# Kernel tuning notes

Measured on AMD Instinct MI355X. Metric: run time of the kernel, lower is better.

Reference implementation:

```python
import jax, jax.numpy as jnp
import numpy as np

N_NODES = 100000
FEATS = 128
N_EDGES = 600000


def setup_inputs() -> dict:
    key = jax.random.key(0)
    ks = jax.random.split(key, 8)
    s = 1.0 / np.sqrt(2 * FEATS)
    s2 = 1.0 / np.sqrt(FEATS)
    return {
        "item_feats": jax.random.normal(ks[0], (N_NODES, FEATS), jnp.float32),
        "user_feats": jax.random.normal(ks[1], (N_NODES, FEATS), jnp.float32),
        "W1": jax.random.uniform(ks[2], (FEATS, 2 * FEATS), jnp.float32, -s, s),
        "b1": jax.random.uniform(ks[3], (FEATS,), jnp.float32, -s, s),
        "W2": jax.random.uniform(ks[4], (1, FEATS), jnp.float32, -s2, s2),
        "b2": jax.random.uniform(ks[5], (1,), jnp.float32, -s2, s2),
        "src_idx": jax.random.randint(ks[6], (N_EDGES,), 0, N_NODES, jnp.int64 if jax.config.jax_enable_x64 else jnp.int32),
        "dst_idx": jax.random.randint(ks[7], (N_EDGES,), 0, N_NODES, jnp.int64 if jax.config.jax_enable_x64 else jnp.int32),
    }


def reference(item_feats, user_feats, W1, b1, W2, b2, src_idx, dst_idx):
    # Per-edge gather + concat: h[e] = [item_feats[src[e]], user_feats[dst[e]]]  -> [E, 2F]
    h = jnp.concatenate([item_feats[src_idx], user_feats[dst_idx]], axis=1)
    # fc1 -> ReLU -> fc2 -> squeeze(1)  (torch Linear: y = x @ W.T + b)
    h1 = jax.nn.relu(h @ W1.T + b1)          # [E, F]
    score = (h1 @ W2.T + b2)[:, 0]           # [E]
    return score
```

## Files before the change

kernel.cpp:

```cpp
#include <hip/hip_runtime.h>
#include <hip/hip_bf16.h>

#define NFEATS 128

typedef __attribute__((ext_vector_type(8))) short bf16x8;
typedef __attribute__((ext_vector_type(4))) float f32x4;
typedef __attribute__((ext_vector_type(4))) short short4v;

__device__ inline short f2bf(float f) {
    union { float f; unsigned u; } c; c.f = f;
    unsigned u = c.u;
    return (short)((u + 0x7FFFu + ((u >> 16) & 1u)) >> 16);
}
__device__ inline float bf2f(short v) {
    union { unsigned u; float f; } c;
    c.u = ((unsigned)(unsigned short)v) << 16;
    return c.f;
}

__global__ __launch_bounds__(512) void precompute_kernel(
    const float* __restrict__ item, const float* __restrict__ user,
    const float* __restrict__ W1, const float* __restrict__ b1,
    short* __restrict__ A, short* __restrict__ B, int n_nodes)
{
    const int which = blockIdx.y;
    const float* __restrict__ X = which ? user : item;
    short* __restrict__ Out = which ? B : A;
    const int k_off4 = which ? 32 : 0;

    __shared__ short Wlds[128][136];
    const int tid = threadIdx.x;

    const float4* W4 = (const float4*)W1;
    for (int i = tid; i < 128 * 32; i += 512) {
        int j = i >> 5, c = i & 31;
        float4 w = W4[j * 64 + k_off4 + c];
        short4v p;
        p[0] = f2bf(w.x); p[1] = f2bf(w.y); p[2] = f2bf(w.z); p[3] = f2bf(w.w);
        *(short4v*)&Wlds[j][c * 4] = p;
    }
    __syncthreads();

    const int wave = tid >> 6, lane = tid & 63;
    const int r16 = lane & 15, q = lane >> 4;
    const int row_base = blockIdx.x * 256 + wave * 32;

    bf16x8 afrag[2][4];
#pragma unroll
    for (int m = 0; m < 2; ++m) {
        int row = row_base + m * 16 + r16;
        if (row >= n_nodes) row = n_nodes - 1;
        const float* xr = X + (size_t)row * NFEATS;
#pragma unroll
        for (int kk = 0; kk < 4; ++kk) {
            int k0 = kk * 32 + q * 8;
            float4 lo = *(const float4*)(xr + k0);
            float4 hi = *(const float4*)(xr + k0 + 4);
            bf16x8 f;
            f[0] = f2bf(lo.x); f[1] = f2bf(lo.y); f[2] = f2bf(lo.z); f[3] = f2bf(lo.w);
            f[4] = f2bf(hi.x); f[5] = f2bf(hi.y); f[6] = f2bf(hi.z); f[7] = f2bf(hi.w);
            afrag[m][kk] = f;
        }
    }

    f32x4 acc[2][8];
#pragma unroll
    for (int n = 0; n < 8; ++n) {
        float bv = which ? 0.f : b1[n * 16 + r16];
        f32x4 init = {bv, bv, bv, bv};
        acc[0][n] = init;
        acc[1][n] = init;
    }

#pragma unroll
    for (int n = 0; n < 8; ++n) {
#pragma unroll
        for (int kk = 0; kk < 4; ++kk) {
            bf16x8 wf = *(const bf16x8*)&Wlds[n * 16 + r16][kk * 32 + q * 8];
            acc[0][n] = __builtin_amdgcn_mfma_f32_16x16x32_bf16(afrag[0][kk], wf, acc[0][n], 0, 0, 0);
            acc[1][n] = __builtin_amdgcn_mfma_f32_16x16x32_bf16(afrag[1][kk], wf, acc[1][n], 0, 0, 0);
        }
    }

#pragma unroll
    for (int m = 0; m < 2; ++m) {
#pragma unroll
        for (int r = 0; r < 4; ++r) {
            int row = row_base + m * 16 + q * 4 + r;
            if (row < n_nodes) {
                short* orow = Out + (size_t)row * NFEATS;
#pragma unroll
                for (int n = 0; n < 8; ++n)
                    orow[n * 16 + r16] = f2bf(acc[m][n][r]);
            }
        }
    }
}

__global__ __launch_bounds__(256) void edge_kernel(
    const short* __restrict__ A, const short* __restrict__ B,
    const int* __restrict__ src, const int* __restrict__ dst,
    const float* __restrict__ W2, const float* __restrict__ b2,
    float* __restrict__ out, int n_edges)
{
    const int t = blockIdx.x * 256 + threadIdx.x;
    const int lane16 = threadIdx.x & 15;

    float w2v[8];
#pragma unroll
    for (int j = 0; j < 8; ++j) w2v[j] = W2[lane16 * 8 + j];
    const float b2v = b2[0];

    const int qw = t >> 4;
    const int nqw = (gridDim.x * 256) >> 4;

    for (int e0 = qw; e0 < n_edges; e0 += 2 * nqw) {
        const int e1 = e0 + nqw;
        const bool has1 = e1 < n_edges;

        int s0 = src[e0], d0 = dst[e0];
        int s1 = has1 ? src[e1] : s0;
        int d1 = has1 ? dst[e1] : d0;

        bf16x8 av0 = *(const bf16x8*)(A + (size_t)s0 * NFEATS + lane16 * 8);
        bf16x8 bv0 = *(const bf16x8*)(B + (size_t)d0 * NFEATS + lane16 * 8);
        bf16x8 av1 = *(const bf16x8*)(A + (size_t)s1 * NFEATS + lane16 * 8);
        bf16x8 bv1 = *(const bf16x8*)(B + (size_t)d1 * NFEATS + lane16 * 8);

        float acc0 = 0.f, acc1 = 0.f;
#pragma unroll
        for (int j = 0; j < 8; ++j) {
            float h0 = bf2f(av0[j]) + bf2f(bv0[j]);
            h0 = fmaxf(h0, 0.f);
            acc0 = fmaf(h0, w2v[j], acc0);
            float h1 = bf2f(av1[j]) + bf2f(bv1[j]);
            h1 = fmaxf(h1, 0.f);
            acc1 = fmaf(h1, w2v[j], acc1);
        }
#pragma unroll
        for (int sh = 1; sh <= 8; sh <<= 1) {
            acc0 += __shfl_xor(acc0, sh);
            acc1 += __shfl_xor(acc1, sh);
        }
        if (lane16 == 0) {
            out[e0] = acc0 + b2v;
            if (has1) out[e1] = acc1 + b2v;
        }
    }
}

extern "C" void kernel_launch(void* const* d_in, const int* in_sizes, int n_in,
                              void* d_out, int out_size, void* d_ws, size_t ws_size,
                              hipStream_t stream) {
    const float* item = (const float*)d_in[0];
    const float* user = (const float*)d_in[1];
    const float* W1   = (const float*)d_in[2];
    const float* b1   = (const float*)d_in[3];
    const float* W2   = (const float*)d_in[4];
    const float* b2   = (const float*)d_in[5];
    const int*   src  = (const int*)d_in[6];
    const int*   dst  = (const int*)d_in[7];
    float* out = (float*)d_out;

    const int n_nodes = in_sizes[0] / NFEATS;
    const int n_edges = in_sizes[6];

    short* A = (short*)d_ws;
    short* B = A + (size_t)n_nodes * NFEATS;

    const int nblk = (n_nodes + 255) / 256;
    dim3 grid(nblk, 2);
    precompute_kernel<<<grid, 512, 0, stream>>>(item, user, W1, b1, A, B, n_nodes);

    edge_kernel<<<2048, 256, 0, stream>>>(A, B, src, dst, W2, b2, out, n_edges);
}
```

Before: 89.07 us.

## Make precompute persistent with double-buffered async global-to-LDS loads

The node precompute GEMM now runs as a persistent grid of 256×2 blocks looping over 64-row tiles. Each block holds its W1 fragments in registers and prefetches the next tile of node features into a second LDS buffer with global_load_lds while it computes the current one. LDS rows are XOR-swizzled to avoid bank conflicts. The aim is to hide global load latency and cut the cost of reloading weights per tile. It relies on async LDS loads being complete at the barrier, and it lowers the work per wave.

```diff
diff --git a/kernel.cpp b/kernel.cpp
--- a/kernel.cpp
+++ b/kernel.cpp
@@ -1,5 +1,6 @@
 #include <hip/hip_runtime.h>
 #include <hip/hip_bf16.h>
+#include <stdint.h>
 
 #define NFEATS 128
 
@@ -18,82 +19,119 @@
     return c.f;
 }
 
-__global__ __launch_bounds__(512) void precompute_kernel(
+__global__ __launch_bounds__(512, 4) void precompute_kernel(
     const float* __restrict__ item, const float* __restrict__ user,
     const float* __restrict__ W1, const float* __restrict__ b1,
     short* __restrict__ A, short* __restrict__ B, int n_nodes)
 {
+    __shared__ __align__(1024) uint8_t lds[34816 + 32768];
+
     const int which = blockIdx.y;
     const float* __restrict__ X = which ? user : item;
     short* __restrict__ Out = which ? B : A;
     const int k_off4 = which ? 32 : 0;
 
-    __shared__ short Wlds[128][136];
     const int tid = threadIdx.x;
-
-    const float4* W4 = (const float4*)W1;
-    for (int i = tid; i < 128 * 32; i += 512) {
-        int j = i >> 5, c = i & 31;
-        float4 w = W4[j * 64 + k_off4 + c];
-        short4v p;
-        p[0] = f2bf(w.x); p[1] = f2bf(w.y); p[2] = f2bf(w.z); p[3] = f2bf(w.w);
-        *(short4v*)&Wlds[j][c * 4] = p;
+    const int w = tid >> 6, lane = tid & 63;
+    const int r16 = lane & 15, q = lane >> 4;
+    const int rowgrp = w >> 1, colhalf = w & 1;
+
+    {
+        short (*Wl)[136] = (short (*)[136])lds;
+        const float4* W4 = (const float4*)W1;
+        for (int i = tid; i < 128 * 32; i += 512) {
+            int j = i >> 5, c = i & 31;
+            float4 wv = W4[j * 64 + k_off4 + c];
+            short4v p;
+            p[0] = f2bf(wv.x); p[1] = f2bf(wv.y); p[2] = f2bf(wv.z); p[3] = f2bf(wv.w);
+            *(short4v*)&Wl[j][c * 4] = p;
+        }
     }
     __syncthreads();
 
-    const int wave = tid >> 6, lane = tid & 63;
-    const int r16 = lane & 15, q = lane >> 4;
-    const int row_base = blockIdx.x * 256 + wave * 32;
-
-    bf16x8 afrag[2][4];
-#pragma unroll
-    for (int m = 0; m < 2; ++m) {
-        int row = row_base + m * 16 + r16;
-        if (row >= n_nodes) row = n_nodes - 1;
-        const float* xr = X + (size_t)row * NFEATS;
+    bf16x8 wfrag[4][4];
+    float bias[4];
+    {
+        short (*Wl)[136] = (short (*)[136])lds;
+#pragma unroll
+        for (int n = 0; n < 4; ++n) {
+            int col = colhalf * 64 + n * 16 + r16;
+#pragma unroll
+            for (int kk = 0; kk < 4; ++kk)
+                wfrag[n][kk] = *(const bf16x8*)&Wl[col][kk * 32 + q * 8];
+            bias[n] = which ? 0.f : b1[col];
+        }
+    }
+    __syncthreads();
+
+    const int n_tiles = (n_nodes + 63) >> 6;
+
+    auto stage = [&](int buf, int t) {
+        uint8_t* base = lds + buf * 34816;
+#pragma unroll
+        for (int i = 0; i < 4; ++i) {
+            int o = (w << 12) + (i << 10) + (lane << 4);
+            int r = o >> 9;
+            int c_lds = (o >> 4) & 31;
+            int node = (t << 6) + r;
+            if (node >= n_nodes) node = n_nodes - 1;
+            const uint8_t* gp = (const uint8_t*)X + (size_t)node * 512
+                              + (size_t)(((c_lds ^ (r & 7)) << 4));
+            auto g1 = (const __attribute__((address_space(1))) uint32_t*)gp;
+            auto l3 = (__attribute__((address_space(3))) uint32_t*)(base + (w << 12) + (i << 10));
+            __builtin_amdgcn_global_load_lds(g1, l3, 16, 0, 0);
+        }
+    };
+
+    int t = blockIdx.x;
+    if (t < n_tiles) stage(0, t);
+    int cur = 0;
+
+    for (; t < n_tiles; t += gridDim.x) {
+        __syncthreads();
+        int tn = t + gridDim.x;
+        if (tn < n_tiles) stage(cur ^ 1, tn);
+
+        const uint8_t* base = lds + cur * 34816;
+        const int r = rowgrp * 16 + r16;
+        const uint8_t* rowp = base + r * 512;
+        const int s = r & 7;
+        bf16x8 afrag[4];
 #pragma unroll
         for (int kk = 0; kk < 4; ++kk) {
-            int k0 = kk * 32 + q * 8;
-            float4 lo = *(const float4*)(xr + k0);
-            float4 hi = *(const float4*)(xr + k0 + 4);
+            int c0 = kk * 8 + q * 2;
+            float4 v0 = *(const float4*)(rowp + ((c0 ^ s) << 4));
+            float4 v1 = *(const float4*)(rowp + (((c0 + 1) ^ s) << 4));
             bf16x8 f;
-            f[0] = f2bf(lo.x); f[1] = f2bf(lo.y); f[2] = f2bf(lo.z); f[3] = f2bf(lo.w);
-            f[4] = f2bf(hi.x); f[5] = f2bf(hi.y); f[6] = f2bf(hi.z); f[7] = f2bf(hi.w);
-            afrag[m][kk] = f;
-        }
-    }
-
-    f32x4 acc[2][8];
-#pragma unroll
-    for (int n = 0; n < 8; ++n) {
-        float bv = which ? 0.f : b1[n * 16 + r16];
-        f32x4 init = {bv, bv, bv, bv};
-        acc[0][n] = init;
-        acc[1][n] = init;
-    }
-
-#pragma unroll
-    for (int n = 0; n < 8; ++n) {
-#pragma unroll
-        for (int kk = 0; kk < 4; ++kk) {
-            bf16x8 wf = *(const bf16x8*)&Wlds[n * 16 + r16][kk * 32 + q * 8];
-            acc[0][n] = __builtin_amdgcn_mfma_f32_16x16x32_bf16(afrag[0][kk], wf, acc[0][n], 0, 0, 0);
-            acc[1][n] = __builtin_amdgcn_mfma_f32_16x16x32_bf16(afrag[1][kk], wf, acc[1][n], 0, 0, 0);
-        }
-    }
-
-#pragma unroll
-    for (int m = 0; m < 2; ++m) {
-#pragma unroll
-        for (int r = 0; r < 4; ++r) {
-            int row = row_base + m * 16 + q * 4 + r;
+            f[0] = f2bf(v0.x); f[1] = f2bf(v0.y); f[2] = f2bf(v0.z); f[3] = f2bf(v0.w);
+            f[4] = f2bf(v1.x); f[5] = f2bf(v1.y); f[6] = f2bf(v1.z); f[7] = f2bf(v1.w);
+            afrag[kk] = f;
+        }
+
+        f32x4 acc[4];
+#pragma unroll
+        for (int n = 0; n < 4; ++n) {
+            f32x4 init = {bias[n], bias[n], bias[n], bias[n]};
+            acc[n] = init;
+        }
+#pragma unroll
+        for (int n = 0; n < 4; ++n)
+#pragma unroll
+            for (int kk = 0; kk < 4; ++kk)
+                acc[n] = __builtin_amdgcn_mfma_f32_16x16x32_bf16(afrag[kk], wfrag[n][kk], acc[n], 0, 0, 0);
+
+        const int row0 = (t << 6) + rowgrp * 16 + q * 4;
+#pragma unroll
+        for (int rr = 0; rr < 4; ++rr) {
+            int row = row0 + rr;
             if (row < n_nodes) {
                 short* orow = Out + (size_t)row * NFEATS;
 #pragma unroll
-                for (int n = 0; n < 8; ++n)
-                    orow[n * 16 + r16] = f2bf(acc[m][n][r]);
+                for (int n = 0; n < 4; ++n)
+                    orow[colhalf * 64 + n * 16 + r16] = f2bf(acc[n][rr]);
             }
         }
+        cur ^= 1;
     }
 }
 
@@ -168,8 +206,7 @@
     short* A = (short*)d_ws;
     short* B = A + (size_t)n_nodes * NFEATS;
 
-    const int nblk = (n_nodes + 255) / 256;
-    dim3 grid(nblk, 2);
+    dim3 grid(256, 2);
     precompute_kernel<<<grid, 512, 0, stream>>>(item, user, W1, b1, A, B, n_nodes);
 
     edge_kernel<<<2048, 256, 0, stream>>>(A, B, src, dst, W2, b2, out, n_edges);
```

Result: faster. 80.58 us (median of 2 runs) (-9.5%).
